# Optimization experiments

Measured on AMD Instinct MI355X. Metric: run time of the kernel, lower is better.

Reference implementation:

```python
import jax, jax.numpy as jnp
import numpy as np
from jax import lax

DIM = 256
NUM_HEADS = 8
SW = 7
HEAD_DIM = DIM // NUM_HEADS
SCALE = HEAD_DIM ** -0.5


def setup_inputs() -> dict:
    key = jax.random.key(0)
    ks = jax.random.split(key, 7)
    B, C, H, W = 8, DIM, 56, 56
    x = jax.random.normal(ks[0], (B, C, H, W), dtype=jnp.float32)
    w_qkv = jax.random.normal(ks[1], (3 * C, C), dtype=jnp.float32) * 0.02
    b_qkv = jnp.zeros((3 * C,), dtype=jnp.float32)
    # depthwise 3x3 kernel, OIHW with feature_group_count=C -> (C,1,3,3)
    w_dw = jax.random.normal(ks[2], (C, 1, 3, 3), dtype=jnp.float32) * 0.02
    b_dw = jnp.zeros((C,), dtype=jnp.float32)
    w_proj = jax.random.normal(ks[3], (C, C), dtype=jnp.float32) * 0.02
    b_proj = jnp.zeros((C,), dtype=jnp.float32)
    return {"x": x, "w_qkv": w_qkv, "b_qkv": b_qkv, "w_dw": w_dw,
            "b_dw": b_dw, "w_proj": w_proj, "b_proj": b_proj}


def _conv1x1(x, w, b):
    # x:[B,C,H,W], w:[O,C] -> [B,O,H,W]
    return jnp.einsum('bchw,oc->bohw', x, w) + b[None, :, None, None]


def _dwconv3x3(x, w, b):
    C = x.shape[1]
    y = lax.conv_general_dilated(x, w, window_strides=(1, 1), padding='SAME',
                                 dimension_numbers=('NCHW', 'OIHW', 'NCHW'),
                                 feature_group_count=C)
    return y + b[None, :, None, None]


def _stripe_attn_H(q, k, v, sw):
    # q,k,v: [B,h,C,H,W]; local attention within sw-thick horizontal stripes
    B, h, C, H, W = q.shape
    sw = min(sw, H)
    pad = (-H) % sw
    if pad:
        pw = [(0, 0)] * 3 + [(0, pad), (0, 0)]
        q = jnp.pad(q, pw); k = jnp.pad(k, pw); v = jnp.pad(v, pw)
    Hp = H + pad
    n = Hp // sw

    def rs(t):
        # -> [B,h,n, sw*W, C]
        return t.reshape(B, h, C, n, sw, W).transpose(0, 1, 3, 4, 5, 2).reshape(B, h, n, sw * W, C)

    qs, ks_, vs = rs(q) * SCALE, rs(k), rs(v)
    attn = jax.nn.softmax(jnp.einsum('bhnqc,bhnkc->bhnqk', qs, ks_), axis=-1)
    out = jnp.einsum('bhnqk,bhnkc->bhnqc', attn, vs)
    out = out.reshape(B, h, n, sw, W, C).transpose(0, 1, 5, 2, 3, 4).reshape(B, h, C, Hp, W)
    return out[:, :, :, :H, :]


def _stripe_attn_W(q, k, v, sw):
    # attention within sw-thick vertical stripes; softmax is permutation-
    # equivariant over the stripe sequence, so transposing H<->W and reusing
    # the H-stripe kernel computes identical math.
    t = lambda a: a.transpose(0, 1, 2, 4, 3)
    return t(_stripe_attn_H(t(q), t(k), t(v), sw))


def reference(x, w_qkv, b_qkv, w_dw, b_dw, w_proj, b_proj):
    B, C, H, W = x.shape
    hh = NUM_HEADS // 2
    qkv = _conv1x1(x, w_qkv, b_qkv)
    q, k, v = jnp.split(qkv, 3, axis=1)
    v = v + _dwconv3x3(v, w_dw, b_dw)

    def heads(t):
        return t.reshape(B, NUM_HEADS, HEAD_DIM, H, W)

    q, k, v = heads(q), heads(k), heads(v)
    out_h = _stripe_attn_H(q[:, :hh], k[:, :hh], v[:, :hh], SW)
    out_w = _stripe_attn_W(q[:, hh:], k[:, hh:], v[:, hh:], SW)
    out = jnp.concatenate([out_h, out_w], axis=1).reshape(B, C, H, W)
    return _conv1x1(out, w_proj, b_proj)
```

## Files before the change

### kernel.cpp

```cpp
#include <hip/hip_runtime.h>
#include <hip/hip_bf16.h>
#include <stdint.h>

#define Bn 8
#define Cn 256
#define Hn 56
#define Wn 56
#define HWn 3136
#define NHEADS 8
#define HDIM 32
#define SEQ 392
#define NSTR 8
#define QKV_LD 768
#define KSC (0.17677669529663689f * 1.4426950408889634f)

#if __has_builtin(__builtin_amdgcn_exp2f)
#define EXP2(x) __builtin_amdgcn_exp2f(x)
#else
#define EXP2(x) exp2f(x)
#endif

typedef short short8 __attribute__((ext_vector_type(8)));
typedef float floatx4 __attribute__((ext_vector_type(4)));

__device__ __forceinline__ unsigned short f2bf(float f) {
  union { float f; uint32_t u; } v; v.f = f;
  uint32_t u = v.u;
  u += 0x7fffu + ((u >> 16) & 1u);
  return (unsigned short)(u >> 16);
}
__device__ __forceinline__ float bf2f(unsigned short h) {
  union { uint32_t u; float f; } v; v.u = ((uint32_t)h) << 16;
  return v.f;
}
__device__ __forceinline__ uint32_t cvt_pk_bf16(float lo, float hi) {
  uint32_t r;
  asm("v_cvt_pk_bf16_f32 %0, %1, %2" : "=v"(r) : "v"(lo), "v"(hi));
  return r;
}
__device__ __forceinline__ void gload16(const unsigned short* g, unsigned short* l) {
  __builtin_amdgcn_global_load_lds((const __attribute__((address_space(1))) void*)g,
                                   (__attribute__((address_space(3))) void*)l, 16, 0, 0);
}

__global__ __launch_bounds__(256) void k_cvt2(const float* __restrict__ a,
                                              const float* __restrict__ b2,
                                              unsigned short* __restrict__ da,
                                              unsigned short* __restrict__ db) {
  int i = blockIdx.x * 256 + threadIdx.x;
  if (i < 49152) {
    float4 v = ((const float4*)a)[i];
    ushort4 o;
    o.x = f2bf(v.x); o.y = f2bf(v.y); o.z = f2bf(v.z); o.w = f2bf(v.w);
    ((ushort4*)da)[i] = o;
  } else {
    int k = i - 49152;
    float4 v = ((const float4*)b2)[k];
    ushort4 o;
    o.x = f2bf(v.x); o.y = f2bf(v.y); o.z = f2bf(v.z); o.w = f2bf(v.w);
    ((ushort4*)db)[k] = o;
  }
}

__global__ __launch_bounds__(256) void k_trans_x(const float* __restrict__ x,
                                                 unsigned short* __restrict__ xt) {
  __shared__ float tile[32][33];
  int pb = blockIdx.x, cb = blockIdx.y, b = blockIdx.z;
  int t = threadIdx.x;
  int c = t >> 3, p4 = (t & 7) * 4;
  float4 v = *(const float4*)(x + (((size_t)b * Cn + cb * 32 + c) * HWn + pb * 32 + p4));
  tile[c][p4 + 0] = v.x; tile[c][p4 + 1] = v.y; tile[c][p4 + 2] = v.z; tile[c][p4 + 3] = v.w;
  __syncthreads();
  int p = t >> 3, c4 = (t & 7) * 4;
  ushort4 o;
  o.x = f2bf(tile[c4 + 0][p]); o.y = f2bf(tile[c4 + 1][p]);
  o.z = f2bf(tile[c4 + 2][p]); o.w = f2bf(tile[c4 + 3][p]);
  *(ushort4*)(xt + (((size_t)b * HWn + pb * 32 + p) * Cn + cb * 32 + c4)) = o;
}

template <int EPI>
__global__ __launch_bounds__(256) void k_gemm(const unsigned short* __restrict__ A,
                                              const unsigned short* __restrict__ Bt,
                                              const float* __restrict__ bias,
                                              unsigned short* __restrict__ outB,
                                              float* __restrict__ outF,
                                              int M, int N, int K, int nx, int nper) {
  __shared__ __align__(16) unsigned short As[2][128 * 64];
  __shared__ __align__(16) unsigned short Bs[2][128 * 64];
  int t = threadIdx.x;
  int raw = blockIdx.x;
  int chunk = gridDim.x >> 3;
  int wg = (raw & 7) * chunk + (raw >> 3);
  int b = wg / nper, r = wg % nper;
  int m0 = (r / nx) * 128, n0 = (r % nx) * 128;
  const unsigned short* Bb = Bt + (size_t)b * N * K;
  int lane = t & 63, w = t >> 6;
  int wr = w >> 1, wc = w & 1;
  int g = lane >> 4, q = lane & 15;
  int srow = w * 32 + (lane >> 3);
  int slot = lane & 7;

  const unsigned short* Ag[4];
  const unsigned short* Bg[4];
  bool bok[4];
  int ldst[4];
#pragma unroll
  for (int i = 0; i < 4; i++) {
    int row = srow + i * 8;
    int cs = slot ^ (row & 7);
    Ag[i] = A + (size_t)(m0 + row) * K + cs * 8;
    int nr = n0 + row;
    bok[i] = (nr < N);
    Bg[i] = Bb + (size_t)(bok[i] ? nr : (N - 1)) * K + cs * 8;
    ldst[i] = (w * 32 + i * 8) * 64;
  }

  floatx4 z4 = {0.f, 0.f, 0.f, 0.f};
  floatx4 acc[4][4];
#pragma unroll
  for (int i = 0; i < 4; i++)
#pragma unroll
    for (int j = 0; j < 4; j++) acc[i][j] = z4;

#pragma unroll
  for (int i = 0; i < 4; i++) gload16(Ag[i], &As[0][ldst[i]]);
#pragma unroll
  for (int i = 0; i < 4; i++) if (bok[i]) gload16(Bg[i], &Bs[0][ldst[i]]);
  asm volatile("s_waitcnt vmcnt(0)" ::: "memory");
  __syncthreads();

  int cur = 0;
  for (int tt = 0; tt < 4; tt++) {
    if (tt < 3) {
      int k0 = (tt + 1) * 64;
#pragma unroll
      for (int i = 0; i < 4; i++) gload16(Ag[i] + k0, &As[cur ^ 1][ldst[i]]);
#pragma unroll
      for (int i = 0; i < 4; i++) if (bok[i]) gload16(Bg[i] + k0, &Bs[cur ^ 1][ldst[i]]);
    }
#pragma unroll
    for (int kk = 0; kk < 64; kk += 32) {
      short8 af[4], bfr[4];
#pragma unroll
      for (int i = 0; i < 4; i++) {
        int row = wr * 64 + i * 16 + q;
        af[i] = *(const short8*)&As[cur][row * 64 + ((((kk >> 3) + g) ^ (q & 7)) << 3)];
      }
#pragma unroll
      for (int j = 0; j < 4; j++) {
        int row = wc * 64 + j * 16 + q;
        bfr[j] = *(const short8*)&Bs[cur][row * 64 + ((((kk >> 3) + g) ^ (q & 7)) << 3)];
      }
#pragma unroll
      for (int i = 0; i < 4; i++)
#pragma unroll
        for (int j = 0; j < 4; j++)
          acc[i][j] = __builtin_amdgcn_mfma_f32_16x16x32_bf16(af[i], bfr[j], acc[i][j], 0, 0, 0);
    }
    if (tt < 3) {
      asm volatile("s_waitcnt vmcnt(0)" ::: "memory");
      __syncthreads();
      cur ^= 1;
    }
  }

#pragma unroll
  for (int i = 0; i < 4; i++) {
    int ob = m0 + wr * 64 + i * 16 + g * 4;
    float bs0 = bias[ob + 0], bs1 = bias[ob + 1], bs2 = bias[ob + 2], bs3 = bias[ob + 3];
    float sc = 1.0f;
    if (EPI == 0 && ob >= 256 && ob < 512) sc = KSC;
#pragma unroll
    for (int j = 0; j < 4; j++) {
      int col = n0 + wc * 64 + j * 16 + q;
      if (col < N) {
        if (EPI == 0) {
          ushort4 o;
          o.x = f2bf((acc[i][j][0] + bs0) * sc);
          o.y = f2bf((acc[i][j][1] + bs1) * sc);
          o.z = f2bf((acc[i][j][2] + bs2) * sc);
          o.w = f2bf((acc[i][j][3] + bs3) * sc);
          *(ushort4*)(outB + ((size_t)b * N + col) * M + ob) = o;
        } else {
          float* po = outF + (size_t)b * M * N;
          po[(size_t)(ob + 0) * N + col] = acc[i][j][0] + bs0;
          po[(size_t)(ob + 1) * N + col] = acc[i][j][1] + bs1;
          po[(size_t)(ob + 2) * N + col] = acc[i][j][2] + bs2;
          po[(size_t)(ob + 3) * N + col] = acc[i][j][3] + bs3;
        }
      }
    }
  }
}

__global__ __launch_bounds__(256) void k_dwconv_t(const unsigned short* __restrict__ qkv,
                                                  const float* __restrict__ wdw,
                                                  const float* __restrict__ bdw,
                                                  unsigned short* __restrict__ vmt,
                                                  unsigned short* __restrict__ qkvw) {
  __shared__ float wS[1152];
  __shared__ float bS[128];
  __shared__ __align__(16) unsigned short tile[16][140];
  int t = threadIdx.x;
  int pass = blockIdx.y, b = blockIdx.z;
  for (int i = t; i < 1152; i += 256) wS[i] = wdw[pass * 1152 + i];
  if (t < 128) bS[t] = bdw[pass * 128 + t];

  int pi = t >> 4, c8 = (t & 15) * 8;
  int i16 = blockIdx.x * 16 + pi;
  int h, w;
  if (pass == 0) { h = i16 / Wn; w = i16 % Wn; }
  else           { w = i16 / Hn; h = i16 % Hn; }

  if (pass == 1) {
    int pi2 = t >> 4, c16 = (t & 15) * 16;
    int ib = blockIdx.x * 16 + pi2;
    int w2 = ib / Hn, h2 = ib % Hn;
    size_t src = ((size_t)b * HWn + h2 * Wn + w2) * QKV_LD;
    int sch = (c16 < 128) ? (128 + c16) : (256 + c16);
    short8 v0 = *(const short8*)(qkv + src + sch);
    short8 v1 = *(const short8*)(qkv + src + sch + 8);
    unsigned short* dst = qkvw + ((size_t)b * HWn + ib) * 256 + c16;
    *(short8*)dst = v0;
    *(short8*)(dst + 8) = v1;
  }
  __syncthreads();

  const unsigned short* vq = qkv + 512 + pass * 128 + c8;
  float a[8];
  short8 vc = *(const short8*)(vq + ((size_t)b * HWn + h * Wn + w) * QKV_LD);
#pragma unroll
  for (int e = 0; e < 8; e++) a[e] = bf2f((unsigned short)vc[e]) + bS[c8 + e];
#pragma unroll
  for (int ky = 0; ky < 3; ky++) {
    int hh = h + ky - 1;
    if (hh < 0 || hh >= Hn) continue;
#pragma unroll
    for (int kx = 0; kx < 3; kx++) {
      int ww = w + kx - 1;
      if (ww < 0 || ww >= Wn) continue;
      short8 vn = *(const short8*)(vq + ((size_t)b * HWn + hh * Wn + ww) * QKV_LD);
#pragma unroll
      for (int e = 0; e < 8; e++) a[e] += bf2f((unsigned short)vn[e]) * wS[(c8 + e) * 9 + ky * 3 + kx];
    }
  }
  short8 o;
#pragma unroll
  for (int e = 0; e < 8; e++) o[e] = (short)f2bf(a[e]);
  *(short8*)&tile[pi][c8] = o;
  __syncthreads();

  int dd = t >> 1, half = t & 1;
  short8 ov;
#pragma unroll
  for (int k2 = 0; k2 < 8; k2++) ov[k2] = (short)tile[half * 8 + k2][dd];
  *(short8*)(vmt + ((size_t)(b * Cn + pass * 128 + dd)) * HWn + blockIdx.x * 16 + half * 8) = ov;
}

__global__ __launch_bounds__(256) void k_attn(const unsigned short* __restrict__ qkv,
                                              const unsigned short* __restrict__ qkvw,
                                              const unsigned short* __restrict__ vmt,
                                              unsigned short* __restrict__ aout) {
  __shared__ __align__(16) unsigned short Ks[12288];
  __shared__ __align__(16) unsigned short Vf[12800];
  __shared__ __align__(16) unsigned short Pf[2048];
  int s = blockIdx.x;
  int hd = blockIdx.y & 7, b = blockIdx.y >> 3;
  int part = blockIdx.z;
  int t = threadIdx.x, lane = t & 63, wv = t >> 6;
  bool wst = (hd >= 4);
  int q = lane & 15, g = lane >> 4;
  int sbase = s * SEQ;

  const unsigned short* base; int ld, qoff, koff;
  if (wst) { base = qkvw + (size_t)b * HWn * 256;    ld = 256;    qoff = (hd - 4) * 32; koff = 128 + (hd - 4) * 32; }
  else     { base = qkv  + (size_t)b * HWn * QKV_LD; ld = QKV_LD; qoff = hd * 32;       koff = 256 + hd * 32; }

  int qb0 = part * 13, qb1 = part ? 25 : 13;

  short8 qpre[4];
#pragma unroll
  for (int it = 0; it < 4; it++) {
    int qb = qb0 + wv + it * 4;
    int qi = qb * 16 + q;
    int qil = (qi < SEQ) ? qi : 391;
    qpre[it] = *(const short8*)(base + qoff + (size_t)(sbase + qil) * ld + g * 8);
  }

  const unsigned short* kgp = base + koff;
#pragma unroll
  for (int P = 0; P < 6; P++) {
    int key = P * 64 + wv * 16 + q;
    int gg = (t >> 4) & 3;
    short8 kv = *(const short8*)(kgp + (size_t)(sbase + key) * ld + gg * 8);
    *(short8*)&Ks[((((key >> 4) * 4 + gg) * 16) + (key & 15)) * 8] = kv;
  }
  short8 kf24;
  {
    int key = 384 + q; if (key > 391) key = 391;
    kf24 = *(const short8*)(kgp + (size_t)(sbase + key) * ld + g * 8);
  }
  const unsigned short* vg = vmt + ((size_t)(b * Cn + hd * HDIM)) * HWn + sbase;
  for (int idx = t; idx < 1600; idx += 256) {
    int d = idx / 50, Gc = idx % 50;
    short8 vv = *(const short8*)(vg + (size_t)d * HWn + Gc * 8);
    *(short8*)&Vf[(Gc * 32 + (d ^ (Gc & 7))) * 8] = vv;
  }
  __syncthreads();

  floatx4 z4 = {0.f, 0.f, 0.f, 0.f};
  unsigned short* Pw = &Pf[wv * 512];
  int gh = g >> 1, ge = (g & 1) * 4;

#pragma unroll
  for (int it = 0; it < 4; it++) {
    int qb = qb0 + wv + it * 4;
    if (qb >= qb1) continue;
    int qi = qb * 16 + q;
    int qil = (qi < SEQ) ? qi : 391;
    short8 qf = qpre[it];

    floatx4 sacc[25];
#pragma unroll
    for (int j = 0; j < 24; j++) {
      short8 kf = *(const short8*)&Ks[((j * 4 + g) * 16 + q) * 8];
      sacc[j] = __builtin_amdgcn_mfma_f32_16x16x32_bf16(kf, qf, z4, 0, 0, 0);
    }
    sacc[24] = __builtin_amdgcn_mfma_f32_16x16x32_bf16(kf24, qf, z4, 0, 0, 0);
    if (g >= 2) { sacc[24][0] = sacc[24][1] = sacc[24][2] = sacc[24][3] = -3.0e38f; }

    float sm = 0.f;
#pragma unroll
    for (int j = 0; j < 25; j++) {
      float e0 = EXP2(sacc[j][0]); float e1 = EXP2(sacc[j][1]);
      float e2 = EXP2(sacc[j][2]); float e3 = EXP2(sacc[j][3]);
      sacc[j][0] = e0; sacc[j][1] = e1; sacc[j][2] = e2; sacc[j][3] = e3;
      sm += (e0 + e1) + (e2 + e3);
    }
    sm += __shfl_xor(sm, 16);
    sm += __shfl_xor(sm, 32);
    float rcp = 1.0f / sm;

#define WRITEP(cc) do {                                                        \
    uint2 wA, wB;                                                              \
    wA.x = cvt_pk_bf16(sacc[2*(cc)][0], sacc[2*(cc)][1]);                      \
    wA.y = cvt_pk_bf16(sacc[2*(cc)][2], sacc[2*(cc)][3]);                      \
    if (2*(cc)+1 < 25) {                                                       \
      wB.x = cvt_pk_bf16(sacc[2*(cc)+1][0], sacc[2*(cc)+1][1]);                \
      wB.y = cvt_pk_bf16(sacc[2*(cc)+1][2], sacc[2*(cc)+1][3]);                \
    } else { wB.x = 0u; wB.y = 0u; }                                           \
    *(uint2*)&Pw[(gh * 16 + q) * 8 + ge] = wA;                                 \
    *(uint2*)&Pw[((2 + gh) * 16 + q) * 8 + ge] = wB;                           \
  } while (0)

    floatx4 o0 = z4, o1 = z4;
    WRITEP(0);
#pragma unroll
    for (int ch = 0; ch < 13; ch++) {
      asm volatile("s_waitcnt lgkmcnt(0)" ::: "memory");
      short8 pfr = *(const short8*)&Pw[(g * 16 + q) * 8];
      int Gc = ch * 4 + g; if (Gc > 49) Gc = 49;
      int sw = Gc & 7;
      short8 vf0 = *(const short8*)&Vf[(Gc * 32 + (q ^ sw)) * 8];
      short8 vf1 = *(const short8*)&Vf[(Gc * 32 + 16 + (q ^ sw)) * 8];
      if (ch < 12) {
        switch (ch + 1) {
          case 1: WRITEP(1); break;  case 2: WRITEP(2); break;
          case 3: WRITEP(3); break;  case 4: WRITEP(4); break;
          case 5: WRITEP(5); break;  case 6: WRITEP(6); break;
          case 7: WRITEP(7); break;  case 8: WRITEP(8); break;
          case 9: WRITEP(9); break;  case 10: WRITEP(10); break;
          case 11: WRITEP(11); break; case 12: WRITEP(12); break;
        }
      }
      o0 = __builtin_amdgcn_mfma_f32_16x16x32_bf16(vf0, pfr, o0, 0, 0, 0);
      o1 = __builtin_amdgcn_mfma_f32_16x16x32_bf16(vf1, pfr, o1, 0, 0, 0);
    }
#undef WRITEP

    if (qi < SEQ) {
      int pq = wst ? ((qil % Wn) * Wn + s * 7 + qil / Wn) : (sbase + qil);
      size_t ob = ((size_t)b * HWn + pq) * Cn + hd * HDIM;
      ushort4 u0, u1;
      u0.x = f2bf(o0[0] * rcp); u0.y = f2bf(o0[1] * rcp);
      u0.z = f2bf(o0[2] * rcp); u0.w = f2bf(o0[3] * rcp);
      u1.x = f2bf(o1[0] * rcp); u1.y = f2bf(o1[1] * rcp);
      u1.z = f2bf(o1[2] * rcp); u1.w = f2bf(o1[3] * rcp);
      *(ushort4*)(aout + ob + g * 4) = u0;
      *(ushort4*)(aout + ob + 16 + g * 4) = u1;
    }
  }
}

extern "C" void kernel_launch(void* const* d_in, const int* in_sizes, int n_in,
                              void* d_out, int out_size, void* d_ws, size_t ws_size,
                              hipStream_t stream) {
  const float* x     = (const float*)d_in[0];
  const float* wqkv  = (const float*)d_in[1];
  const float* bqkv  = (const float*)d_in[2];
  const float* wdw   = (const float*)d_in[3];
  const float* bdw   = (const float*)d_in[4];
  const float* wproj = (const float*)d_in[5];
  const float* bproj = (const float*)d_in[6];
  float* out = (float*)d_out;

  unsigned short* xt   = (unsigned short*)d_ws;
  unsigned short* wqb  = xt + (size_t)Bn * HWn * Cn;
  unsigned short* wpb  = wqb + 768 * 256;
  unsigned short* qkvb = wpb + 256 * 256;
  unsigned short* vmt  = qkvb + (size_t)Bn * HWn * QKV_LD;
  unsigned short* aout = vmt + (size_t)Bn * HWn * Cn;
  unsigned short* qkvw = aout + (size_t)Bn * HWn * Cn;

  k_cvt2<<<dim3(256), 256, 0, stream>>>(wqkv, wproj, wqb, wpb);
  k_trans_x<<<dim3(98, 8, Bn), 256, 0, stream>>>(x, xt);
  k_gemm<0><<<dim3(1200), 256, 0, stream>>>(wqb, xt, bqkv, qkvb, nullptr, 768, HWn, 256, 25, 150);
  k_dwconv_t<<<dim3(196, 2, Bn), 256, 0, stream>>>(qkvb, wdw, bdw, vmt, qkvw);
  k_attn<<<dim3(NSTR, Bn * NHEADS, 2), 256, 0, stream>>>(qkvb, qkvw, vmt, aout);
  k_gemm<1><<<dim3(400), 256, 0, stream>>>(wpb, aout, bproj, nullptr, out, 256, HWn, 256, 25, 50);
}
```

Baseline: 109.6 us.

## Stage GEMM epilogues through LDS and merge attention query halves into one block

Both GEMM epilogues now go through shared memory, a swizzled bf16 tile for the QKV GEMM and a padded fp32 tile for the projection. Each thread then writes contiguous 16-byte rows instead of scattered 8-byte or 4-byte stores. The tile ordering now iterates M fastest so neighbouring blocks share the same activation columns. The attention kernel drops the two-part z-split and uses 512-thread blocks, so K/V are loaded once per stripe instead of twice, at the cost of fewer, larger blocks and more LDS per block.

```diff
diff --git a/kernel.cpp b/kernel.cpp
--- a/kernel.cpp
+++ b/kernel.cpp
@@ -84,15 +84,16 @@
                                               const float* __restrict__ bias,
                                               unsigned short* __restrict__ outB,
                                               float* __restrict__ outF,
-                                              int M, int N, int K, int nx, int nper) {
-  __shared__ __align__(16) unsigned short As[2][128 * 64];
-  __shared__ __align__(16) unsigned short Bs[2][128 * 64];
+                                              int M, int N, int K, int nm, int nper) {
+  __shared__ __align__(16) char SH[EPI ? 67584 : 65536];
+  unsigned short* As = (unsigned short*)SH;
+  unsigned short* Bs = As + 16384;
   int t = threadIdx.x;
   int raw = blockIdx.x;
   int chunk = gridDim.x >> 3;
   int wg = (raw & 7) * chunk + (raw >> 3);
   int b = wg / nper, r = wg % nper;
-  int m0 = (r / nx) * 128, n0 = (r % nx) * 128;
+  int m0 = (r % nm) * 128, n0 = (r / nm) * 128;
   const unsigned short* Bb = Bt + (size_t)b * N * K;
   int lane = t & 63, w = t >> 6;
   int wr = w >> 1, wc = w & 1;
@@ -123,9 +124,9 @@
     for (int j = 0; j < 4; j++) acc[i][j] = z4;
 
 #pragma unroll
-  for (int i = 0; i < 4; i++) gload16(Ag[i], &As[0][ldst[i]]);
-#pragma unroll
-  for (int i = 0; i < 4; i++) if (bok[i]) gload16(Bg[i], &Bs[0][ldst[i]]);
+  for (int i = 0; i < 4; i++) gload16(Ag[i], &As[ldst[i]]);
+#pragma unroll
+  for (int i = 0; i < 4; i++) if (bok[i]) gload16(Bg[i], &Bs[ldst[i]]);
   asm volatile("s_waitcnt vmcnt(0)" ::: "memory");
   __syncthreads();
 
@@ -133,23 +134,25 @@
   for (int tt = 0; tt < 4; tt++) {
     if (tt < 3) {
       int k0 = (tt + 1) * 64;
-#pragma unroll
-      for (int i = 0; i < 4; i++) gload16(Ag[i] + k0, &As[cur ^ 1][ldst[i]]);
-#pragma unroll
-      for (int i = 0; i < 4; i++) if (bok[i]) gload16(Bg[i] + k0, &Bs[cur ^ 1][ldst[i]]);
-    }
+      int nb = (cur ^ 1) * 8192;
+#pragma unroll
+      for (int i = 0; i < 4; i++) gload16(Ag[i] + k0, &As[nb + ldst[i]]);
+#pragma unroll
+      for (int i = 0; i < 4; i++) if (bok[i]) gload16(Bg[i] + k0, &Bs[nb + ldst[i]]);
+    }
+    int cb = cur * 8192;
 #pragma unroll
     for (int kk = 0; kk < 64; kk += 32) {
       short8 af[4], bfr[4];
 #pragma unroll
       for (int i = 0; i < 4; i++) {
         int row = wr * 64 + i * 16 + q;
-        af[i] = *(const short8*)&As[cur][row * 64 + ((((kk >> 3) + g) ^ (q & 7)) << 3)];
+        af[i] = *(const short8*)&As[cb + row * 64 + ((((kk >> 3) + g) ^ (q & 7)) << 3)];
       }
 #pragma unroll
       for (int j = 0; j < 4; j++) {
         int row = wc * 64 + j * 16 + q;
-        bfr[j] = *(const short8*)&Bs[cur][row * 64 + ((((kk >> 3) + g) ^ (q & 7)) << 3)];
+        bfr[j] = *(const short8*)&Bs[cb + row * 64 + ((((kk >> 3) + g) ^ (q & 7)) << 3)];
       }
 #pragma unroll
       for (int i = 0; i < 4; i++)
@@ -164,30 +167,62 @@
     }
   }
 
-#pragma unroll
-  for (int i = 0; i < 4; i++) {
-    int ob = m0 + wr * 64 + i * 16 + g * 4;
-    float bs0 = bias[ob + 0], bs1 = bias[ob + 1], bs2 = bias[ob + 2], bs3 = bias[ob + 3];
-    float sc = 1.0f;
-    if (EPI == 0 && ob >= 256 && ob < 512) sc = KSC;
-#pragma unroll
-    for (int j = 0; j < 4; j++) {
-      int col = n0 + wc * 64 + j * 16 + q;
-      if (col < N) {
-        if (EPI == 0) {
-          ushort4 o;
-          o.x = f2bf((acc[i][j][0] + bs0) * sc);
-          o.y = f2bf((acc[i][j][1] + bs1) * sc);
-          o.z = f2bf((acc[i][j][2] + bs2) * sc);
-          o.w = f2bf((acc[i][j][3] + bs3) * sc);
-          *(ushort4*)(outB + ((size_t)b * N + col) * M + ob) = o;
-        } else {
-          float* po = outF + (size_t)b * M * N;
-          po[(size_t)(ob + 0) * N + col] = acc[i][j][0] + bs0;
-          po[(size_t)(ob + 1) * N + col] = acc[i][j][1] + bs1;
-          po[(size_t)(ob + 2) * N + col] = acc[i][j][2] + bs2;
-          po[(size_t)(ob + 3) * N + col] = acc[i][j][3] + bs3;
-        }
+  __syncthreads();
+  if (EPI == 0) {
+    unsigned short* E = (unsigned short*)SH;
+#pragma unroll
+    for (int i = 0; i < 4; i++) {
+      int ob = m0 + wr * 64 + i * 16 + g * 4;
+      float bs0 = bias[ob + 0], bs1 = bias[ob + 1], bs2 = bias[ob + 2], bs3 = bias[ob + 3];
+      float sc = (ob >= 256 && ob < 512) ? KSC : 1.0f;
+      int lobg = wr * 8 + i * 2 + (g >> 1);
+#pragma unroll
+      for (int j = 0; j < 4; j++) {
+        int lc = wc * 64 + j * 16 + q;
+        ushort4 o;
+        o.x = f2bf((acc[i][j][0] + bs0) * sc);
+        o.y = f2bf((acc[i][j][1] + bs1) * sc);
+        o.z = f2bf((acc[i][j][2] + bs2) * sc);
+        o.w = f2bf((acc[i][j][3] + bs3) * sc);
+        *(ushort4*)&E[lc * 128 + ((lobg ^ (lc & 7)) << 3) + (g & 1) * 4] = o;
+      }
+    }
+    __syncthreads();
+    int c = t >> 1, hh = t & 1;
+    int col = n0 + c;
+    if (col < N) {
+      unsigned short* dst = outB + ((size_t)b * N + col) * M + m0 + hh * 64;
+#pragma unroll
+      for (int k2 = 0; k2 < 8; k2++) {
+        short8 v = *(const short8*)&E[c * 128 + (((hh * 8 + k2) ^ (c & 7)) << 3)];
+        *(short8*)(dst + k2 * 8) = v;
+      }
+    }
+  } else {
+    float* Ef = (float*)SH;
+#pragma unroll
+    for (int i = 0; i < 4; i++) {
+      int ob = m0 + wr * 64 + i * 16 + g * 4;
+      int lob = wr * 64 + i * 16 + g * 4;
+      float bs0 = bias[ob + 0], bs1 = bias[ob + 1], bs2 = bias[ob + 2], bs3 = bias[ob + 3];
+#pragma unroll
+      for (int j = 0; j < 4; j++) {
+        int lc = wc * 64 + j * 16 + q;
+        Ef[(lob + 0) * 132 + lc] = acc[i][j][0] + bs0;
+        Ef[(lob + 1) * 132 + lc] = acc[i][j][1] + bs1;
+        Ef[(lob + 2) * 132 + lc] = acc[i][j][2] + bs2;
+        Ef[(lob + 3) * 132 + lc] = acc[i][j][3] + bs3;
+      }
+    }
+    __syncthreads();
+    int rr = t >> 1, hh = t & 1;
+    int cb2 = n0 + hh * 64;
+    if (cb2 < N) {
+      float* dst = outF + (size_t)b * M * N + (size_t)(m0 + rr) * N + cb2;
+#pragma unroll
+      for (int k2 = 0; k2 < 16; k2++) {
+        float4 v = *(const float4*)&Ef[rr * 132 + hh * 64 + k2 * 4];
+        *(float4*)(dst + k2 * 4) = v;
       }
     }
   }
@@ -257,16 +292,15 @@
   *(short8*)(vmt + ((size_t)(b * Cn + pass * 128 + dd)) * HWn + blockIdx.x * 16 + half * 8) = ov;
 }
 
-__global__ __launch_bounds__(256) void k_attn(const unsigned short* __restrict__ qkv,
+__global__ __launch_bounds__(512) void k_attn(const unsigned short* __restrict__ qkv,
                                               const unsigned short* __restrict__ qkvw,
                                               const unsigned short* __restrict__ vmt,
                                               unsigned short* __restrict__ aout) {
   __shared__ __align__(16) unsigned short Ks[12288];
   __shared__ __align__(16) unsigned short Vf[12800];
-  __shared__ __align__(16) unsigned short Pf[2048];
+  __shared__ __align__(16) unsigned short Pf[4096];
   int s = blockIdx.x;
   int hd = blockIdx.y & 7, b = blockIdx.y >> 3;
-  int part = blockIdx.z;
   int t = threadIdx.x, lane = t & 63, wv = t >> 6;
   bool wst = (hd >= 4);
   int q = lane & 15, g = lane >> 4;
@@ -276,12 +310,10 @@
   if (wst) { base = qkvw + (size_t)b * HWn * 256;    ld = 256;    qoff = (hd - 4) * 32; koff = 128 + (hd - 4) * 32; }
   else     { base = qkv  + (size_t)b * HWn * QKV_LD; ld = QKV_LD; qoff = hd * 32;       koff = 256 + hd * 32; }
 
-  int qb0 = part * 13, qb1 = part ? 25 : 13;
-
   short8 qpre[4];
 #pragma unroll
   for (int it = 0; it < 4; it++) {
-    int qb = qb0 + wv + it * 4;
+    int qb = it * 8 + wv;
     int qi = qb * 16 + q;
     int qil = (qi < SEQ) ? qi : 391;
     qpre[it] = *(const short8*)(base + qoff + (size_t)(sbase + qil) * ld + g * 8);
@@ -289,9 +321,9 @@
 
   const unsigned short* kgp = base + koff;
 #pragma unroll
-  for (int P = 0; P < 6; P++) {
-    int key = P * 64 + wv * 16 + q;
-    int gg = (t >> 4) & 3;
+  for (int P = 0; P < 3; P++) {
+    int key = P * 128 + (t >> 2);
+    int gg = t & 3;
     short8 kv = *(const short8*)(kgp + (size_t)(sbase + key) * ld + gg * 8);
     *(short8*)&Ks[((((key >> 4) * 4 + gg) * 16) + (key & 15)) * 8] = kv;
   }
@@ -301,7 +333,7 @@
     kf24 = *(const short8*)(kgp + (size_t)(sbase + key) * ld + g * 8);
   }
   const unsigned short* vg = vmt + ((size_t)(b * Cn + hd * HDIM)) * HWn + sbase;
-  for (int idx = t; idx < 1600; idx += 256) {
+  for (int idx = t; idx < 1600; idx += 512) {
     int d = idx / 50, Gc = idx % 50;
     short8 vv = *(const short8*)(vg + (size_t)d * HWn + Gc * 8);
     *(short8*)&Vf[(Gc * 32 + (d ^ (Gc & 7))) * 8] = vv;
@@ -314,8 +346,8 @@
 
 #pragma unroll
   for (int it = 0; it < 4; it++) {
-    int qb = qb0 + wv + it * 4;
-    if (qb >= qb1) continue;
+    int qb = it * 8 + wv;
+    if (qb >= 25) continue;
     int qi = qb * 16 + q;
     int qil = (qi < SEQ) ? qi : 391;
     short8 qf = qpre[it];
@@ -414,8 +446,8 @@
 
   k_cvt2<<<dim3(256), 256, 0, stream>>>(wqkv, wproj, wqb, wpb);
   k_trans_x<<<dim3(98, 8, Bn), 256, 0, stream>>>(x, xt);
-  k_gemm<0><<<dim3(1200), 256, 0, stream>>>(wqb, xt, bqkv, qkvb, nullptr, 768, HWn, 256, 25, 150);
+  k_gemm<0><<<dim3(1200), 256, 0, stream>>>(wqb, xt, bqkv, qkvb, nullptr, 768, HWn, 256, 6, 150);
   k_dwconv_t<<<dim3(196, 2, Bn), 256, 0, stream>>>(qkvb, wdw, bdw, vmt, qkvw);
-  k_attn<<<dim3(NSTR, Bn * NHEADS, 2), 256, 0, stream>>>(qkvb, qkvw, vmt, aout);
-  k_gemm<1><<<dim3(400), 256, 0, stream>>>(wpb, aout, bproj, nullptr, out, 256, HWn, 256, 25, 50);
-}
+  k_attn<<<dim3(NSTR, Bn * NHEADS), 512, 0, stream>>>(qkvb, qkvw, vmt, aout);
+  k_gemm<1><<<dim3(400), 256, 0, stream>>>(wpb, aout, bproj, nullptr, out, 256, HWn, 256, 2, 50);
+}
```

Measured after the change: 111.4 us. About the same (+1.6%).
